# Kernel optimization log

Measured on AMD Instinct MI355X. Metric: run time of the kernel, lower is better.

## Reference

```python
import jax, jax.numpy as jnp
import numpy as np

B, L, SIZE, BACK, H = 4, 1024, 1024, 512, 16
D = SIZE // H  # head_size = 64


def setup_inputs() -> dict:
    key = jax.random.key(0)
    ks = jax.random.split(key, 18)
    s = 0.02
    return {
        "k": jax.random.normal(ks[0], (B, L, SIZE), jnp.float32),
        "v": jax.random.normal(ks[1], (B, L, SIZE), jnp.float32),
        "q": jax.random.normal(ks[2], (B, L, SIZE), jnp.float32),
        "background": jax.random.normal(ks[3], (B, L, BACK), jnp.float32),
        # weights stored [in, out] (pre-transposed vs torch Linear)
        "Wk": jax.random.normal(ks[4], (SIZE, SIZE), jnp.float32) * s,
        "bk": jnp.zeros((SIZE,), jnp.float32),
        "Wv": jax.random.normal(ks[5], (SIZE, SIZE), jnp.float32) * s,
        "bv": jnp.zeros((SIZE,), jnp.float32),
        "Wq": jax.random.normal(ks[6], (SIZE, SIZE), jnp.float32) * s,
        "bq": jnp.zeros((SIZE,), jnp.float32),
        "Wb": jax.random.normal(ks[7], (BACK, SIZE), jnp.float32) * s,
        "bb": jnp.zeros((SIZE,), jnp.float32),
        "Wo": jax.random.normal(ks[8], (SIZE, SIZE), jnp.float32) * s,
        "bo": jnp.zeros((SIZE,), jnp.float32),
    }


def _heads(x):
    # [B, L, H*D] -> [B, H, L, D]
    b, l, _ = x.shape
    return x.reshape(b, l, H, D).transpose(0, 2, 1, 3)


def reference(k, v, q, background, Wk, bk, Wv, bv, Wq, bq, Wb, bb, Wo, bo):
    kh = _heads(k @ Wk + bk)
    vh = _heads(v @ Wv + bv)
    qh = _heads(q @ Wq + bq) / jnp.sqrt(jnp.asarray(D, k.dtype))
    gh = _heads(background @ Wb + bb)
    scores = jnp.einsum("bhqd,bhkd->bhqk", qh, kh)   # [B,H,Lq,Lk]
    gates = jax.nn.sigmoid(jnp.einsum("bhqd,bhkd->bhqk", qh, gh))
    attn = jax.nn.softmax(scores, axis=-1) * gates    # dropout = identity (eval)
    ctx = jnp.einsum("bhqk,bhkd->bhqd", attn, vh)
    ctx = ctx.transpose(0, 2, 1, 3).reshape(k.shape[0], -1, H * D)
    return ctx @ Wo + bo
```

## Files before the change

kernel.cpp:

```cpp
#include <hip/hip_runtime.h>
#include <cstddef>
#include <cstdint>

typedef __attribute__((ext_vector_type(8))) short s16x8;
typedef __attribute__((ext_vector_type(4))) short s16x4;
typedef __attribute__((ext_vector_type(4))) float f32x4;

#define MFMA(a, b, c) __builtin_amdgcn_mfma_f32_16x16x32_bf16(a, b, c, 0, 0, 0)
#define LOG2E 1.44269504088896f

__device__ __forceinline__ short f2bf(float x) {
    uint32_t u = __float_as_uint(x);
    u = (u + 0x7FFFu + ((u >> 16) & 1u)) >> 16;
    return (short)u;
}

__device__ __forceinline__ void gld16(const void* g, void* l) {
    __builtin_amdgcn_global_load_lds(
        (const __attribute__((address_space(1))) unsigned int*)g,
        (__attribute__((address_space(3))) unsigned int*)l, 16, 0, 0);
}

__device__ __forceinline__ float fexp2(float x) {
#if __has_builtin(__builtin_amdgcn_exp2f)
    return __builtin_amdgcn_exp2f(x);
#else
    return exp2f(x);
#endif
}

__device__ __forceinline__ float frcp(float x) {
#if __has_builtin(__builtin_amdgcn_rcpf)
    return __builtin_amdgcn_rcpf(x);
#else
    return 1.f / x;
#endif
}

__device__ __forceinline__ unsigned cvtpk(float lo, float hi) {
    unsigned r;
    asm("v_cvt_pk_bf16_f32 %0, %1, %2" : "=v"(r) : "v"(lo), "v"(hi));
    return r;
}

struct ConvP { const float* in[4]; short* out[4]; };

__global__ __launch_bounds__(256)
void conv_all(ConvP p) {
    const int i = blockIdx.x * 256 + threadIdx.x;
    int r, base;
    if (i < 524288)            { r = 0; base = 0; }
    else if (i < 1048576)      { r = 1; base = 524288; }
    else if (i < 1310720)      { r = 2; base = 1048576; }
    else                       { r = 3; base = 1310720; }
    const int j = i - base;
    const float4 a = *(const float4*)(p.in[r] + (size_t)j * 8);
    const float4 b = *(const float4*)(p.in[r] + (size_t)j * 8 + 4);
    s16x8 o;
    o[0] = f2bf(a.x); o[1] = f2bf(a.y); o[2] = f2bf(a.z); o[3] = f2bf(a.w);
    o[4] = f2bf(b.x); o[5] = f2bf(b.y); o[6] = f2bf(b.z); o[7] = f2bf(b.w);
    *(s16x8*)(p.out[r] + (size_t)j * 8) = o;
}

struct WtP { const float* W[5]; short* Wt[5]; int K[5]; };

__global__ __launch_bounds__(256)
void conv_wt_b(WtP p) {
    __shared__ float T[64][65];
    const int z = blockIdx.z;
    const int K = p.K[z];
    const int k0 = blockIdx.y << 6, n0 = blockIdx.x << 6;
    if (k0 >= K) return;
    const float* W = p.W[z];
    short* Wt = p.Wt[z];
    const int tr = threadIdx.x >> 4, tc4 = (threadIdx.x & 15) << 2;
    #pragma unroll
    for (int i = 0; i < 4; ++i) {
        const int r = tr + i * 16;
        const float4 v = *(const float4*)(W + (size_t)(k0 + r) * 1024 + n0 + tc4);
        T[r][tc4 + 0] = v.x; T[r][tc4 + 1] = v.y;
        T[r][tc4 + 2] = v.z; T[r][tc4 + 3] = v.w;
    }
    __syncthreads();
    #pragma unroll
    for (int i = 0; i < 4; ++i) {
        const int nr = tr + i * 16;
        s16x4 o;
        o[0] = f2bf(T[tc4 + 0][nr]); o[1] = f2bf(T[tc4 + 1][nr]);
        o[2] = f2bf(T[tc4 + 2][nr]); o[3] = f2bf(T[tc4 + 3][nr]);
        *(s16x4*)(Wt + (size_t)(n0 + nr) * K + k0 + tc4) = o;
    }
}

struct Proj5P {
    const short* A[5]; const short* Bt[5]; const float* bias[5];
    void* Y[5]; int Kd[5]; float alpha[5]; int mode[5];
};

__global__ __launch_bounds__(256, 2)
void proj_gemm128d(Proj5P p, int zbase) {
    __shared__ __align__(16) short lds[2 * 16384];

    const int tid = threadIdx.x;
    const int w = tid >> 6, lane = tid & 63;
    const int la = lane & 15, kg = lane >> 4;
    const int wr = w >> 1, wc = w & 1;

    const int cpx = gridDim.x >> 3;
    const int orig = blockIdx.x;
    const int swz = (orig & 7) * cpx + (orig >> 3);
    const int z = zbase + (swz >> 8);
    const int rem = swz & 255;
    const int bm = rem >> 3, bn = rem & 7;

    const short* __restrict__ A  = p.A[z];
    const short* __restrict__ Bt = p.Bt[z];
    const int K = p.Kd[z];
    const int NT = K >> 6;

    const int srow = tid >> 3;
    const int csrc = (tid & 7) ^ (srow & 7);
    const short* gA = A  + (size_t)(bm * 128 + srow) * K + csrc * 8;
    const short* gB = Bt + (size_t)(bn * 128 + srow) * K + csrc * 8;
    short* dstA = &lds[srow * 64 + (tid & 7) * 8];
    short* dstB = dstA + 8192;

#define STAGE(t, nb) do {                                                  \
        const size_t ko_ = (size_t)((t) << 6);                             \
        short* ba_ = dstA + (nb) * 16384;                                  \
        short* bb_ = dstB + (nb) * 16384;                                  \
        _Pragma("unroll")                                                  \
        for (int i = 0; i < 4; ++i) {                                      \
            gld16(gA + (size_t)(32 * i) * K + ko_, ba_ + i * 2048);        \
            gld16(gB + (size_t)(32 * i) * K + ko_, bb_ + i * 2048);       \
        }                                                                  \
    } while (0)

    const int c0 = kg ^ (la & 7), c1 = (4 + kg) ^ (la & 7);
    const int aRd = (wr * 64 + la) * 64;
    const int bRd = 8192 + (wc * 64 + la) * 64;

    f32x4 acc[4][4] = {};

    STAGE(0, 0);
    asm volatile("s_waitcnt vmcnt(0)" ::: "memory");
    asm volatile("s_barrier" ::: "memory");

    for (int t = 0; t < NT; ++t) {
        const int cb = (t & 1) * 16384;
        if (t + 1 < NT) STAGE(t + 1, (t & 1) ^ 1);
        s16x8 af[4][2], bf[4][2];
        #pragma unroll
        for (int m = 0; m < 4; ++m) {
            af[m][0] = *(const s16x8*)&lds[cb + aRd + m * 1024 + c0 * 8];
            af[m][1] = *(const s16x8*)&lds[cb + aRd + m * 1024 + c1 * 8];
        }
        #pragma unroll
        for (int n = 0; n < 4; ++n) {
            bf[n][0] = *(const s16x8*)&lds[cb + bRd + n * 1024 + c0 * 8];
            bf[n][1] = *(const s16x8*)&lds[cb + bRd + n * 1024 + c1 * 8];
        }
        __builtin_amdgcn_s_setprio(1);
        #pragma unroll
        for (int m = 0; m < 4; ++m)
            #pragma unroll
            for (int n = 0; n < 4; ++n) {
                acc[m][n] = MFMA(af[m][0], bf[n][0], acc[m][n]);
                acc[m][n] = MFMA(af[m][1], bf[n][1], acc[m][n]);
            }
        __builtin_amdgcn_s_setprio(0);
        if (t + 1 < NT) {
            asm volatile("s_waitcnt vmcnt(0)" ::: "memory");
            asm volatile("s_barrier" ::: "memory");
        }
    }
#undef STAGE

    const float* __restrict__ bias = p.bias[z];
    const float alpha = p.alpha[z];
    const int mode = p.mode[z];

    if (mode == 2) {
        short* __restrict__ Y = (short*)p.Y[z];
        short* Tv = lds;
        asm volatile("s_waitcnt lgkmcnt(0)" ::: "memory");
        asm volatile("s_barrier" ::: "memory");
        #pragma unroll
        for (int ni = 0; ni < 4; ++ni) {
            const int rrow = wc * 64 + ni * 16 + la;
            const float bs = bias[bn * 128 + rrow];
            #pragma unroll
            for (int mi = 0; mi < 4; ++mi) {
                const int l0 = wr * 64 + mi * 16 + kg * 4;
                const unsigned d0 = cvtpk(alpha * (acc[mi][ni][0] + bs),
                                          alpha * (acc[mi][ni][1] + bs));
                const unsigned d1 = cvtpk(alpha * (acc[mi][ni][2] + bs),
                                          alpha * (acc[mi][ni][3] + bs));
                *(unsigned*)&Tv[rrow * 132 + l0]     = d0;
                *(unsigned*)&Tv[rrow * 132 + l0 + 2] = d1;
            }
        }
        asm volatile("s_barrier" ::: "memory");
        const int bb_ = (bm * 128) >> 10;
        const int l0g = (bm * 128) & 1023;
        #pragma unroll
        for (int s = 0; s < 8; ++s) {
            const int c = tid + (s << 8);
            const int rr = c >> 4, seg = c & 15;
            const int hh = bn * 2 + (rr >> 6), dd = rr & 63;
            const s16x8 vv = *(const s16x8*)&Tv[rr * 132 + seg * 8];
            *(s16x8*)&Y[((((size_t)bb_ * 16 + hh) * 64 + dd) << 10) + l0g + seg * 8] = vv;
        }
        return;
    }

    #pragma unroll
    for (int n = 0; n < 4; ++n) {
        const int col = bn * 128 + wc * 64 + n * 16 + la;
        const float bs = bias[col];
        #pragma unroll
        for (int m = 0; m < 4; ++m) {
            const int row0 = bm * 128 + wr * 64 + m * 16 + kg * 4;
            #pragma unroll
            for (int r = 0; r < 4; ++r) {
                const float v = alpha * (acc[m][n][r] + bs);
                if (mode == 0) {
                    ((short*)p.Y[z])[(size_t)(row0 + r) * 1024 + col] = f2bf(v);
                } else {
                    ((float*)p.Y[z])[(size_t)(row0 + r) * 1024 + col] = v;
                }
            }
        }
    }
}

__global__ __launch_bounds__(512)
void attn_mfma(const short* __restrict__ qh, const short* __restrict__ kh,
               const short* __restrict__ gh, const short* __restrict__ vt,
               short* __restrict__ ctx) {
    __shared__ __align__(16) short lds[33792];

    const int tid = threadIdx.x, w = tid >> 6, lane = tid & 63;
    const int la = lane & 15, kg = lane >> 4;

    const int orig = blockIdx.x;
    const int xcd = orig & 7, i = orig >> 3;
    const int bh = xcd * 8 + (i >> 3);
    const int qt = i & 7;
    const int b = bh >> 4, h = bh & 15;
    const int q0 = qt << 7;

    const size_t hb = ((size_t)b << 20) + ((size_t)h << 6);
    const size_t vtbase = ((size_t)bh) << 16;

    const int qrow = q0 + w * 16 + la;
    const s16x8 aq0 = *(const s16x8*)(qh + hb + (size_t)qrow * 1024 + kg * 8);
    const s16x8 aq1 = *(const s16x8*)(qh + hb + (size_t)qrow * 1024 + 32 + kg * 8);

    const int sr = tid >> 3, sc = tid & 7;
    const int cs = sc ^ (sr & 7);
    const short* ksrc = kh + hb + (size_t)sr * 1024 + cs * 8;
    const short* gsrc = gh + hb + (size_t)sr * 1024 + cs * 8;
    const short* vsrc = vt + vtbase + (size_t)sr * 1024 + cs * 8;
    const int sdst = tid * 8;

    const int ch0 = (kg ^ (la & 7)) * 8;
    const int ch1 = ((4 + kg) ^ (la & 7)) * 8;
    const int pbase = 24576 + w * 1152;

    float s_run = 0.f;
    f32x4 o[4] = {};

#define ASTG(kt, bb) do {                                                  \
        const size_t kr_ = (size_t)((kt) << 6) * 1024;                     \
        gld16(ksrc + kr_, &lds[(bb) * 4096 + sdst]);                       \
        gld16(gsrc + kr_, &lds[8192 + (bb) * 4096 + sdst]);                \
        gld16(vsrc + ((kt) << 6), &lds[16384 + (bb) * 4096 + sdst]);       \
    } while (0)

    ASTG(0, 0);
    asm volatile("s_waitcnt vmcnt(0)" ::: "memory");
    asm volatile("s_barrier" ::: "memory");

    for (int kt = 0; kt < 16; ++kt) {
        const int cb = (kt & 1) * 4096;
        if (kt < 15) ASTG(kt + 1, (kt + 1) & 1);

        f32x4 st[4] = {}, gt[4] = {};
        #pragma unroll
        for (int nf = 0; nf < 4; ++nf) {
            const int rb = cb + (nf * 16 + la) * 64;
            const s16x8 kb0 = *(const s16x8*)&lds[rb + ch0];
            const s16x8 kb1 = *(const s16x8*)&lds[rb + ch1];
            st[nf] = MFMA(kb0, aq0, st[nf]);
            st[nf] = MFMA(kb1, aq1, st[nf]);
            const s16x8 gb0 = *(const s16x8*)&lds[8192 + rb + ch0];
            const s16x8 gb1 = *(const s16x8*)&lds[8192 + rb + ch1];
            gt[nf] = MFMA(gb0, aq0, gt[nf]);
            gt[nf] = MFMA(gb1, aq1, gt[nf]);
        }

        float ps = 0.f;
        unsigned pkw[4][2];
        #pragma unroll
        for (int nf = 0; nf < 4; ++nf) {
            const float p0 = fexp2(st[nf][0]);
            const float p1 = fexp2(st[nf][1]);
            const float p2 = fexp2(st[nf][2]);
            const float p3 = fexp2(st[nf][3]);
            ps += (p0 + p1) + (p2 + p3);
            const float g0 = frcp(1.f + fexp2(-gt[nf][0]));
            const float g1 = frcp(1.f + fexp2(-gt[nf][1]));
            const float g2 = frcp(1.f + fexp2(-gt[nf][2]));
            const float g3 = frcp(1.f + fexp2(-gt[nf][3]));
            pkw[nf][0] = cvtpk(p0 * g0, p1 * g1);
            pkw[nf][1] = cvtpk(p2 * g2, p3 * g3);
        }
        s_run += ps;

        #pragma unroll
        for (int nf = 0; nf < 4; ++nf) {
            *(unsigned*)&lds[pbase + la * 72 + nf * 16 + kg * 4]     = pkw[nf][0];
            *(unsigned*)&lds[pbase + la * 72 + nf * 16 + kg * 4 + 2] = pkw[nf][1];
        }

        const s16x8 pa0 = *(const s16x8*)&lds[pbase + la * 72 + kg * 8];
        const s16x8 pa1 = *(const s16x8*)&lds[pbase + la * 72 + 32 + kg * 8];
        #pragma unroll
        for (int nf = 0; nf < 4; ++nf) {
            const int rb = cb + (nf * 16 + la) * 64;
            const s16x8 vb0 = *(const s16x8*)&lds[16384 + rb + ch0];
            const s16x8 vb1 = *(const s16x8*)&lds[16384 + rb + ch1];
            o[nf] = MFMA(vb0, pa0, o[nf]);
            o[nf] = MFMA(vb1, pa1, o[nf]);
        }

        if (kt < 15) {
            asm volatile("s_waitcnt vmcnt(0)" ::: "memory");
            asm volatile("s_barrier" ::: "memory");
        }
    }
#undef ASTG

    float sv = s_run;
    sv += __shfl_xor(sv, 16);
    sv += __shfl_xor(sv, 32);
    const float inv = frcp(sv);
    short* crow = ctx + ((size_t)(b * 1024 + qrow) << 10) + (h << 6);
    #pragma unroll
    for (int nf = 0; nf < 4; ++nf) {
        *(unsigned*)(crow + nf * 16 + kg * 4)     = cvtpk(o[nf][0] * inv, o[nf][1] * inv);
        *(unsigned*)(crow + nf * 16 + kg * 4 + 2) = cvtpk(o[nf][2] * inv, o[nf][3] * inv);
    }
}

extern "C" void kernel_launch(void* const* d_in, const int* in_sizes, int n_in,
                              void* d_out, int out_size, void* d_ws, size_t ws_size,
                              hipStream_t stream) {
    (void)in_sizes; (void)n_in; (void)out_size; (void)ws_size;

    const float* k  = (const float*)d_in[0];
    const float* v  = (const float*)d_in[1];
    const float* q  = (const float*)d_in[2];
    const float* bg = (const float*)d_in[3];
    const float* Wk = (const float*)d_in[4];  const float* bk = (const float*)d_in[5];
    const float* Wv = (const float*)d_in[6];  const float* bv = (const float*)d_in[7];
    const float* Wq = (const float*)d_in[8];  const float* bq = (const float*)d_in[9];
    const float* Wb = (const float*)d_in[10]; const float* bb = (const float*)d_in[11];
    const float* Wo = (const float*)d_in[12]; const float* bo = (const float*)d_in[13];

    short* ws = (short*)d_ws;
    const size_t MN = (size_t)4096 * 1024;
    short* khb = ws;
    short* qhb = ws + MN;
    short* ghb = ws + 2 * MN;
    short* vtb = ws + 3 * MN;
    short* xk  = ws + 4 * MN;
    short* xq  = ws + 5 * MN;
    short* xg  = ws + 6 * MN;
    short* xv  = ws + 6 * MN + MN / 2;
    short* wkt = ws + 7 * MN + MN / 2;
    short* wvt = wkt + 1048576;
    short* wqt = wvt + 1048576;
    short* wot = wqt + 1048576;
    short* wbt = wot + 1048576;
    short* ctxb = xk;

    const dim3 blk(256);

    WtP wp;
    wp.W[0] = Wk; wp.Wt[0] = wkt; wp.K[0] = 1024;
    wp.W[1] = Wv; wp.Wt[1] = wvt; wp.K[1] = 1024;
    wp.W[2] = Wq; wp.Wt[2] = wqt; wp.K[2] = 1024;
    wp.W[3] = Wb; wp.Wt[3] = wbt; wp.K[3] = 512;
    wp.W[4] = Wo; wp.Wt[4] = wot; wp.K[4] = 1024;
    conv_wt_b<<<dim3(16, 16, 5), blk, 0, stream>>>(wp);

    ConvP cp;
    cp.in[0] = k;  cp.out[0] = xk;
    cp.in[1] = q;  cp.out[1] = xq;
    cp.in[2] = bg; cp.out[2] = xg;
    cp.in[3] = v;  cp.out[3] = xv;
    conv_all<<<7168, blk, 0, stream>>>(cp);

    Proj5P p5;
    p5.A[0] = xk;   p5.Bt[0] = wkt; p5.bias[0] = bk; p5.Y[0] = khb;
    p5.Kd[0] = 1024; p5.alpha[0] = LOG2E;  p5.mode[0] = 0;
    p5.A[1] = xq;   p5.Bt[1] = wqt; p5.bias[1] = bq; p5.Y[1] = qhb;
    p5.Kd[1] = 1024; p5.alpha[1] = 0.125f; p5.mode[1] = 0;
    p5.A[2] = xg;   p5.Bt[2] = wbt; p5.bias[2] = bb; p5.Y[2] = ghb;
    p5.Kd[2] = 512;  p5.alpha[2] = LOG2E;  p5.mode[2] = 0;
    p5.A[3] = xv;   p5.Bt[3] = wvt; p5.bias[3] = bv; p5.Y[3] = vtb;
    p5.Kd[3] = 1024; p5.alpha[3] = 1.0f;   p5.mode[3] = 2;
    p5.A[4] = ctxb; p5.Bt[4] = wot; p5.bias[4] = bo; p5.Y[4] = d_out;
    p5.Kd[4] = 1024; p5.alpha[4] = 1.0f;   p5.mode[4] = 1;

    proj_gemm128d<<<dim3(1024), blk, 0, stream>>>(p5, 0);

    attn_mfma<<<dim3(512), dim3(512), 0, stream>>>(qhb, khb, ghb, vtb, ctxb);

    proj_gemm128d<<<dim3(256), blk, 0, stream>>>(p5, 4);
}
```

Measured before the change: 118.6 us.

## Replace double-buffered K=64 GEMM pipeline with 4-stage K=32 pipeline

The projection GEMM now stages K-tiles of 32 instead of 64 and uses a four-slot LDS ring with three tiles in flight, waiting with partial vmcnt instead of draining all loads each step. The aim is to hide global-to-LDS latency better and avoid a full vmcnt(0) stall per iteration, while keeping total LDS the same. It trades this for twice as many barriers and smaller MFMA batches per barrier, and it changes the LDS swizzle for the 32-wide rows.

```diff
diff --git a/kernel.cpp b/kernel.cpp
--- a/kernel.cpp
+++ b/kernel.cpp
@@ -98,8 +98,8 @@
 };
 
 __global__ __launch_bounds__(256, 2)
-void proj_gemm128d(Proj5P p, int zbase) {
-    __shared__ __align__(16) short lds[2 * 16384];
+void proj_gemm128p(Proj5P p, int zbase) {
+    __shared__ __align__(16) short lds[4 * 8192];
 
     const int tid = threadIdx.x;
     const int w = tid >> 6, lane = tid & 63;
@@ -116,65 +116,63 @@
     const short* __restrict__ A  = p.A[z];
     const short* __restrict__ Bt = p.Bt[z];
     const int K = p.Kd[z];
-    const int NT = K >> 6;
-
-    const int srow = tid >> 3;
-    const int csrc = (tid & 7) ^ (srow & 7);
+    const int NT = K >> 5;
+
+    const int srow = tid >> 2;
+    const int csrc = (tid & 3) ^ ((tid >> 3) & 3);
     const short* gA = A  + (size_t)(bm * 128 + srow) * K + csrc * 8;
     const short* gB = Bt + (size_t)(bn * 128 + srow) * K + csrc * 8;
-    short* dstA = &lds[srow * 64 + (tid & 7) * 8];
-    short* dstB = dstA + 8192;
-
-#define STAGE(t, nb) do {                                                  \
-        const size_t ko_ = (size_t)((t) << 6);                             \
-        short* ba_ = dstA + (nb) * 16384;                                  \
-        short* bb_ = dstB + (nb) * 16384;                                  \
+    const int d0 = tid * 8;
+
+#define STAGE(t) do {                                                      \
+        const int bq_ = ((t) & 3) * 8192;                                  \
+        const size_t ko_ = (size_t)((t) << 5);                             \
+        gld16(gA + ko_,                  &lds[bq_ + d0]);                  \
+        gld16(gA + (size_t)64 * K + ko_, &lds[bq_ + 2048 + d0]);           \
+        gld16(gB + ko_,                  &lds[bq_ + 4096 + d0]);           \
+        gld16(gB + (size_t)64 * K + ko_, &lds[bq_ + 6144 + d0]);           \
+    } while (0)
+
+    const int cr = (kg ^ ((la >> 1) & 3)) * 8;
+    const int aRd = (wr * 64 + la) * 32 + cr;
+    const int bRd = 4096 + (wc * 64 + la) * 32 + cr;
+
+    f32x4 acc[4][4] = {};
+
+#define TILE_BODY(t) do {                                                  \
+        const int cb_ = ((t) & 3) * 8192;                                  \
+        s16x8 af[4], bf[4];                                                \
         _Pragma("unroll")                                                  \
-        for (int i = 0; i < 4; ++i) {                                      \
-            gld16(gA + (size_t)(32 * i) * K + ko_, ba_ + i * 2048);        \
-            gld16(gB + (size_t)(32 * i) * K + ko_, bb_ + i * 2048);       \
-        }                                                                  \
+        for (int m = 0; m < 4; ++m)                                        \
+            af[m] = *(const s16x8*)&lds[cb_ + aRd + m * 512];              \
+        _Pragma("unroll")                                                  \
+        for (int n = 0; n < 4; ++n)                                        \
+            bf[n] = *(const s16x8*)&lds[cb_ + bRd + n * 512];              \
+        __builtin_amdgcn_s_setprio(1);                                     \
+        _Pragma("unroll")                                                  \
+        for (int m = 0; m < 4; ++m)                                        \
+            _Pragma("unroll")                                              \
+            for (int n = 0; n < 4; ++n)                                    \
+                acc[m][n] = MFMA(af[m], bf[n], acc[m][n]);                 \
+        __builtin_amdgcn_s_setprio(0);                                     \
     } while (0)
 
-    const int c0 = kg ^ (la & 7), c1 = (4 + kg) ^ (la & 7);
-    const int aRd = (wr * 64 + la) * 64;
-    const int bRd = 8192 + (wc * 64 + la) * 64;
-
-    f32x4 acc[4][4] = {};
-
-    STAGE(0, 0);
+    STAGE(0); STAGE(1); STAGE(2);
+
+    for (int t = 0; t < NT - 2; ++t) {
+        asm volatile("s_waitcnt vmcnt(8)" ::: "memory");
+        asm volatile("s_barrier" ::: "memory");
+        TILE_BODY(t);
+        if (t + 3 < NT) STAGE(t + 3);
+    }
+    asm volatile("s_waitcnt vmcnt(4)" ::: "memory");
+    asm volatile("s_barrier" ::: "memory");
+    TILE_BODY(NT - 2);
     asm volatile("s_waitcnt vmcnt(0)" ::: "memory");
     asm volatile("s_barrier" ::: "memory");
-
-    for (int t = 0; t < NT; ++t) {
-        const int cb = (t & 1) * 16384;
-        if (t + 1 < NT) STAGE(t + 1, (t & 1) ^ 1);
-        s16x8 af[4][2], bf[4][2];
-        #pragma unroll
-        for (int m = 0; m < 4; ++m) {
-            af[m][0] = *(const s16x8*)&lds[cb + aRd + m * 1024 + c0 * 8];
-            af[m][1] = *(const s16x8*)&lds[cb + aRd + m * 1024 + c1 * 8];
-        }
-        #pragma unroll
-        for (int n = 0; n < 4; ++n) {
-            bf[n][0] = *(const s16x8*)&lds[cb + bRd + n * 1024 + c0 * 8];
-            bf[n][1] = *(const s16x8*)&lds[cb + bRd + n * 1024 + c1 * 8];
-        }
-        __builtin_amdgcn_s_setprio(1);
-        #pragma unroll
-        for (int m = 0; m < 4; ++m)
-            #pragma unroll
-            for (int n = 0; n < 4; ++n) {
-                acc[m][n] = MFMA(af[m][0], bf[n][0], acc[m][n]);
-                acc[m][n] = MFMA(af[m][1], bf[n][1], acc[m][n]);
-            }
-        __builtin_amdgcn_s_setprio(0);
-        if (t + 1 < NT) {
-            asm volatile("s_waitcnt vmcnt(0)" ::: "memory");
-            asm volatile("s_barrier" ::: "memory");
-        }
-    }
+    TILE_BODY(NT - 1);
 #undef STAGE
+#undef TILE_BODY
 
     const float* __restrict__ bias = p.bias[z];
     const float alpha = p.alpha[z];
@@ -192,12 +190,12 @@
             #pragma unroll
             for (int mi = 0; mi < 4; ++mi) {
                 const int l0 = wr * 64 + mi * 16 + kg * 4;
-                const unsigned d0 = cvtpk(alpha * (acc[mi][ni][0] + bs),
-                                          alpha * (acc[mi][ni][1] + bs));
-                const unsigned d1 = cvtpk(alpha * (acc[mi][ni][2] + bs),
-                                          alpha * (acc[mi][ni][3] + bs));
-                *(unsigned*)&Tv[rrow * 132 + l0]     = d0;
-                *(unsigned*)&Tv[rrow * 132 + l0 + 2] = d1;
+                const unsigned dd0 = cvtpk(alpha * (acc[mi][ni][0] + bs),
+                                           alpha * (acc[mi][ni][1] + bs));
+                const unsigned dd1 = cvtpk(alpha * (acc[mi][ni][2] + bs),
+                                           alpha * (acc[mi][ni][3] + bs));
+                *(unsigned*)&Tv[rrow * 132 + l0]     = dd0;
+                *(unsigned*)&Tv[rrow * 132 + l0 + 2] = dd1;
             }
         }
         asm volatile("s_barrier" ::: "memory");
@@ -415,9 +413,9 @@
     p5.A[4] = ctxb; p5.Bt[4] = wot; p5.bias[4] = bo; p5.Y[4] = d_out;
     p5.Kd[4] = 1024; p5.alpha[4] = 1.0f;   p5.mode[4] = 1;
 
-    proj_gemm128d<<<dim3(1024), blk, 0, stream>>>(p5, 0);
+    proj_gemm128p<<<dim3(1024), blk, 0, stream>>>(p5, 0);
 
     attn_mfma<<<dim3(512), dim3(512), 0, stream>>>(qhb, khb, ghb, vtb, ctxb);
 
-    proj_gemm128d<<<dim3(256), blk, 0, stream>>>(p5, 4);
-}
+    proj_gemm128p<<<dim3(256), blk, 0, stream>>>(p5, 4);
+}
```

After: 124.1 us. +4.6%, slower.

## Process 256 query rows per attention block, halving grid and K/G/V reloads

Applied to the files above, without the earlier changes.

Each attention workgroup now handles 256 query rows instead of 128: each wave owns two 16-row query groups, and each K/G/V tile staged in LDS is reused for both. The grid halves from 512 to 256 blocks, so K, G and V are streamed from global memory half as often. The cost is more registers per wave for the doubled accumulators and Q fragments, and only 256 blocks for 256 CUs, so each CU gets about one block with longer serial work and less latency hiding. Launch bounds now request 4 waves per SIMD.

```diff
diff --git a/kernel.cpp b/kernel.cpp
--- a/kernel.cpp
+++ b/kernel.cpp
@@ -234,7 +234,7 @@
     }
 }
 
-__global__ __launch_bounds__(512)
+__global__ __launch_bounds__(512, 4)
 void attn_mfma(const short* __restrict__ qh, const short* __restrict__ kh,
                const short* __restrict__ gh, const short* __restrict__ vt,
                short* __restrict__ ctx) {
@@ -245,17 +245,21 @@
 
     const int orig = blockIdx.x;
     const int xcd = orig & 7, i = orig >> 3;
-    const int bh = xcd * 8 + (i >> 3);
-    const int qt = i & 7;
+    const int bh = xcd * 8 + (i >> 2);
+    const int qt = i & 3;
     const int b = bh >> 4, h = bh & 15;
-    const int q0 = qt << 7;
+    const int q0 = qt << 8;
 
     const size_t hb = ((size_t)b << 20) + ((size_t)h << 6);
     const size_t vtbase = ((size_t)bh) << 16;
 
-    const int qrow = q0 + w * 16 + la;
-    const s16x8 aq0 = *(const s16x8*)(qh + hb + (size_t)qrow * 1024 + kg * 8);
-    const s16x8 aq1 = *(const s16x8*)(qh + hb + (size_t)qrow * 1024 + 32 + kg * 8);
+    s16x8 aq[2][2];
+    #pragma unroll
+    for (int g = 0; g < 2; ++g) {
+        const int qr = q0 + w * 32 + g * 16 + la;
+        aq[g][0] = *(const s16x8*)(qh + hb + (size_t)qr * 1024 + kg * 8);
+        aq[g][1] = *(const s16x8*)(qh + hb + (size_t)qr * 1024 + 32 + kg * 8);
+    }
 
     const int sr = tid >> 3, sc = tid & 7;
     const int cs = sc ^ (sr & 7);
@@ -268,8 +272,8 @@
     const int ch1 = ((4 + kg) ^ (la & 7)) * 8;
     const int pbase = 24576 + w * 1152;
 
-    float s_run = 0.f;
-    f32x4 o[4] = {};
+    float s_run[2] = {0.f, 0.f};
+    f32x4 o[2][4] = {};
 
 #define ASTG(kt, bb) do {                                                  \
         const size_t kr_ = (size_t)((kt) << 6) * 1024;                     \
@@ -286,53 +290,56 @@
         const int cb = (kt & 1) * 4096;
         if (kt < 15) ASTG(kt + 1, (kt + 1) & 1);
 
-        f32x4 st[4] = {}, gt[4] = {};
-        #pragma unroll
-        for (int nf = 0; nf < 4; ++nf) {
-            const int rb = cb + (nf * 16 + la) * 64;
-            const s16x8 kb0 = *(const s16x8*)&lds[rb + ch0];
-            const s16x8 kb1 = *(const s16x8*)&lds[rb + ch1];
-            st[nf] = MFMA(kb0, aq0, st[nf]);
-            st[nf] = MFMA(kb1, aq1, st[nf]);
-            const s16x8 gb0 = *(const s16x8*)&lds[8192 + rb + ch0];
-            const s16x8 gb1 = *(const s16x8*)&lds[8192 + rb + ch1];
-            gt[nf] = MFMA(gb0, aq0, gt[nf]);
-            gt[nf] = MFMA(gb1, aq1, gt[nf]);
-        }
-
-        float ps = 0.f;
-        unsigned pkw[4][2];
-        #pragma unroll
-        for (int nf = 0; nf < 4; ++nf) {
-            const float p0 = fexp2(st[nf][0]);
-            const float p1 = fexp2(st[nf][1]);
-            const float p2 = fexp2(st[nf][2]);
-            const float p3 = fexp2(st[nf][3]);
-            ps += (p0 + p1) + (p2 + p3);
-            const float g0 = frcp(1.f + fexp2(-gt[nf][0]));
-            const float g1 = frcp(1.f + fexp2(-gt[nf][1]));
-            const float g2 = frcp(1.f + fexp2(-gt[nf][2]));
-            const float g3 = frcp(1.f + fexp2(-gt[nf][3]));
-            pkw[nf][0] = cvtpk(p0 * g0, p1 * g1);
-            pkw[nf][1] = cvtpk(p2 * g2, p3 * g3);
-        }
-        s_run += ps;
-
-        #pragma unroll
-        for (int nf = 0; nf < 4; ++nf) {
-            *(unsigned*)&lds[pbase + la * 72 + nf * 16 + kg * 4]     = pkw[nf][0];
-            *(unsigned*)&lds[pbase + la * 72 + nf * 16 + kg * 4 + 2] = pkw[nf][1];
-        }
-
-        const s16x8 pa0 = *(const s16x8*)&lds[pbase + la * 72 + kg * 8];
-        const s16x8 pa1 = *(const s16x8*)&lds[pbase + la * 72 + 32 + kg * 8];
-        #pragma unroll
-        for (int nf = 0; nf < 4; ++nf) {
-            const int rb = cb + (nf * 16 + la) * 64;
-            const s16x8 vb0 = *(const s16x8*)&lds[16384 + rb + ch0];
-            const s16x8 vb1 = *(const s16x8*)&lds[16384 + rb + ch1];
-            o[nf] = MFMA(vb0, pa0, o[nf]);
-            o[nf] = MFMA(vb1, pa1, o[nf]);
+        #pragma unroll
+        for (int g = 0; g < 2; ++g) {
+            f32x4 st[4] = {}, gt[4] = {};
+            #pragma unroll
+            for (int nf = 0; nf < 4; ++nf) {
+                const int rb = cb + (nf * 16 + la) * 64;
+                const s16x8 kb0 = *(const s16x8*)&lds[rb + ch0];
+                const s16x8 kb1 = *(const s16x8*)&lds[rb + ch1];
+                st[nf] = MFMA(kb0, aq[g][0], st[nf]);
+                st[nf] = MFMA(kb1, aq[g][1], st[nf]);
+                const s16x8 gb0 = *(const s16x8*)&lds[8192 + rb + ch0];
+                const s16x8 gb1 = *(const s16x8*)&lds[8192 + rb + ch1];
+                gt[nf] = MFMA(gb0, aq[g][0], gt[nf]);
+                gt[nf] = MFMA(gb1, aq[g][1], gt[nf]);
+            }
+
+            float ps = 0.f;
+            unsigned pkw[4][2];
+            #pragma unroll
+            for (int nf = 0; nf < 4; ++nf) {
+                const float p0 = fexp2(st[nf][0]);
+                const float p1 = fexp2(st[nf][1]);
+                const float p2 = fexp2(st[nf][2]);
+                const float p3 = fexp2(st[nf][3]);
+                ps += (p0 + p1) + (p2 + p3);
+                const float g0 = frcp(1.f + fexp2(-gt[nf][0]));
+                const float g1 = frcp(1.f + fexp2(-gt[nf][1]));
+                const float g2 = frcp(1.f + fexp2(-gt[nf][2]));
+                const float g3 = frcp(1.f + fexp2(-gt[nf][3]));
+                pkw[nf][0] = cvtpk(p0 * g0, p1 * g1);
+                pkw[nf][1] = cvtpk(p2 * g2, p3 * g3);
+            }
+            s_run[g] += ps;
+
+            #pragma unroll
+            for (int nf = 0; nf < 4; ++nf) {
+                *(unsigned*)&lds[pbase + la * 72 + nf * 16 + kg * 4]     = pkw[nf][0];
+                *(unsigned*)&lds[pbase + la * 72 + nf * 16 + kg * 4 + 2] = pkw[nf][1];
+            }
+
+            const s16x8 pa0 = *(const s16x8*)&lds[pbase + la * 72 + kg * 8];
+            const s16x8 pa1 = *(const s16x8*)&lds[pbase + la * 72 + 32 + kg * 8];
+            #pragma unroll
+            for (int nf = 0; nf < 4; ++nf) {
+                const int rb = cb + (nf * 16 + la) * 64;
+                const s16x8 vb0 = *(const s16x8*)&lds[16384 + rb + ch0];
+                const s16x8 vb1 = *(const s16x8*)&lds[16384 + rb + ch1];
+                o[g][nf] = MFMA(vb0, pa0, o[g][nf]);
+                o[g][nf] = MFMA(vb1, pa1, o[g][nf]);
+            }
         }
 
         if (kt < 15) {
@@ -342,15 +349,19 @@
     }
 #undef ASTG
 
-    float sv = s_run;
-    sv += __shfl_xor(sv, 16);
-    sv += __shfl_xor(sv, 32);
-    const float inv = frcp(sv);
-    short* crow = ctx + ((size_t)(b * 1024 + qrow) << 10) + (h << 6);
     #pragma unroll
-    for (int nf = 0; nf < 4; ++nf) {
-        *(unsigned*)(crow + nf * 16 + kg * 4)     = cvtpk(o[nf][0] * inv, o[nf][1] * inv);
-        *(unsigned*)(crow + nf * 16 + kg * 4 + 2) = cvtpk(o[nf][2] * inv, o[nf][3] * inv);
+    for (int g = 0; g < 2; ++g) {
+        float sv = s_run[g];
+        sv += __shfl_xor(sv, 16);
+        sv += __shfl_xor(sv, 32);
+        const float inv = frcp(sv);
+        const int qr = q0 + w * 32 + g * 16 + la;
+        short* crow = ctx + ((size_t)(b * 1024 + qr) << 10) + (h << 6);
+        #pragma unroll
+        for (int nf = 0; nf < 4; ++nf) {
+            *(unsigned*)(crow + nf * 16 + kg * 4)     = cvtpk(o[g][nf][0] * inv, o[g][nf][1] * inv);
+            *(unsigned*)(crow + nf * 16 + kg * 4 + 2) = cvtpk(o[g][nf][2] * inv, o[g][nf][3] * inv);
+        }
     }
 }
 
@@ -417,7 +428,7 @@
 
     proj_gemm128d<<<dim3(1024), blk, 0, stream>>>(p5, 0);
 
-    attn_mfma<<<dim3(512), dim3(512), 0, stream>>>(qhb, khb, ghb, vtb, ctxb);
+    attn_mfma<<<dim3(256), dim3(512), 0, stream>>>(qhb, khb, ghb, vtb, ctxb);
 
     proj_gemm128d<<<dim3(256), blk, 0, stream>>>(p5, 4);
 }
```

Result: slower. 132.9 us (+12.0%).

## Fuse fp32-to-bf16 activation conversion into projection GEMM A-tile staging

Applied to the files above, without the earlier changes.

Removes the standalone conversion kernel that turned the k/q/v/background inputs into bf16 buffers. The projection GEMM now loads fp32 A tiles into registers, packs them to bf16 and writes them to LDS after the wait, while B still uses async global-to-LDS loads. This avoids a full extra read/write pass over the activations, but adds register pressure and serialized conversion and LDS stores in the GEMM main loop, with double the global bytes for the A operand.

```diff
diff --git a/kernel.cpp b/kernel.cpp
--- a/kernel.cpp
+++ b/kernel.cpp
@@ -5,6 +5,7 @@
 typedef __attribute__((ext_vector_type(8))) short s16x8;
 typedef __attribute__((ext_vector_type(4))) short s16x4;
 typedef __attribute__((ext_vector_type(4))) float f32x4;
+typedef __attribute__((ext_vector_type(4))) unsigned u32x4;
 
 #define MFMA(a, b, c) __builtin_amdgcn_mfma_f32_16x16x32_bf16(a, b, c, 0, 0, 0)
 #define LOG2E 1.44269504088896f
@@ -41,25 +42,6 @@
     unsigned r;
     asm("v_cvt_pk_bf16_f32 %0, %1, %2" : "=v"(r) : "v"(lo), "v"(hi));
     return r;
-}
-
-struct ConvP { const float* in[4]; short* out[4]; };
-
-__global__ __launch_bounds__(256)
-void conv_all(ConvP p) {
-    const int i = blockIdx.x * 256 + threadIdx.x;
-    int r, base;
-    if (i < 524288)            { r = 0; base = 0; }
-    else if (i < 1048576)      { r = 1; base = 524288; }
-    else if (i < 1310720)      { r = 2; base = 1048576; }
-    else                       { r = 3; base = 1310720; }
-    const int j = i - base;
-    const float4 a = *(const float4*)(p.in[r] + (size_t)j * 8);
-    const float4 b = *(const float4*)(p.in[r] + (size_t)j * 8 + 4);
-    s16x8 o;
-    o[0] = f2bf(a.x); o[1] = f2bf(a.y); o[2] = f2bf(a.z); o[3] = f2bf(a.w);
-    o[4] = f2bf(b.x); o[5] = f2bf(b.y); o[6] = f2bf(b.z); o[7] = f2bf(b.w);
-    *(s16x8*)(p.out[r] + (size_t)j * 8) = o;
 }
 
 struct WtP { const float* W[5]; short* Wt[5]; int K[5]; };
@@ -93,10 +75,13 @@
 }
 
 struct Proj5P {
-    const short* A[5]; const short* Bt[5]; const float* bias[5];
+    const float* Af[5];
+    const short* A[5];
+    const short* Bt[5]; const float* bias[5];
     void* Y[5]; int Kd[5]; float alpha[5]; int mode[5];
 };
 
+template <int F32A>
 __global__ __launch_bounds__(256, 2)
 void proj_gemm128d(Proj5P p, int zbase) {
     __shared__ __align__(16) short lds[2 * 16384];
@@ -113,26 +98,46 @@
     const int rem = swz & 255;
     const int bm = rem >> 3, bn = rem & 7;
 
-    const short* __restrict__ A  = p.A[z];
-    const short* __restrict__ Bt = p.Bt[z];
     const int K = p.Kd[z];
     const int NT = K >> 6;
 
     const int srow = tid >> 3;
     const int csrc = (tid & 7) ^ (srow & 7);
-    const short* gA = A  + (size_t)(bm * 128 + srow) * K + csrc * 8;
-    const short* gB = Bt + (size_t)(bn * 128 + srow) * K + csrc * 8;
+    const float* gAf = p.Af[z] ? p.Af[z] + (size_t)(bm * 128 + srow) * K + csrc * 8 : nullptr;
+    const short* gA  = p.A[z]  ? p.A[z]  + (size_t)(bm * 128 + srow) * K + csrc * 8 : nullptr;
+    const short* gB  = p.Bt[z] + (size_t)(bn * 128 + srow) * K + csrc * 8;
     short* dstA = &lds[srow * 64 + (tid & 7) * 8];
     short* dstB = dstA + 8192;
 
-#define STAGE(t, nb) do {                                                  \
+    float4 av[4][2];
+
+#define STAGE_ISSUE(t, nb) do {                                            \
         const size_t ko_ = (size_t)((t) << 6);                             \
-        short* ba_ = dstA + (nb) * 16384;                                  \
         short* bb_ = dstB + (nb) * 16384;                                  \
         _Pragma("unroll")                                                  \
         for (int i = 0; i < 4; ++i) {                                      \
-            gld16(gA + (size_t)(32 * i) * K + ko_, ba_ + i * 2048);        \
-            gld16(gB + (size_t)(32 * i) * K + ko_, bb_ + i * 2048);       \
+            if (F32A) {                                                    \
+                av[i][0] = *(const float4*)(gAf + (size_t)(32 * i) * K + ko_);     \
+                av[i][1] = *(const float4*)(gAf + (size_t)(32 * i) * K + ko_ + 4); \
+            } else {                                                       \
+                gld16(gA + (size_t)(32 * i) * K + ko_,                     \
+                      dstA + (nb) * 16384 + i * 2048);                     \
+            }                                                              \
+            gld16(gB + (size_t)(32 * i) * K + ko_, bb_ + i * 2048);        \
+        }                                                                  \
+    } while (0)
+
+#define A_WRITE(nb) do {                                                   \
+        if (F32A) {                                                        \
+            _Pragma("unroll")                                              \
+            for (int i = 0; i < 4; ++i) {                                  \
+                u32x4 pk;                                                  \
+                pk[0] = cvtpk(av[i][0].x, av[i][0].y);                     \
+                pk[1] = cvtpk(av[i][0].z, av[i][0].w);                     \
+                pk[2] = cvtpk(av[i][1].x, av[i][1].y);                     \
+                pk[3] = cvtpk(av[i][1].z, av[i][1].w);                     \
+                *(u32x4*)(dstA + (nb) * 16384 + i * 2048) = pk;            \
+            }                                                              \
         }                                                                  \
     } while (0)
 
@@ -142,13 +147,16 @@
 
     f32x4 acc[4][4] = {};
 
-    STAGE(0, 0);
+    STAGE_ISSUE(0, 0);
     asm volatile("s_waitcnt vmcnt(0)" ::: "memory");
+    A_WRITE(0);
+    asm volatile("s_waitcnt lgkmcnt(0)" ::: "memory");
     asm volatile("s_barrier" ::: "memory");
 
     for (int t = 0; t < NT; ++t) {
         const int cb = (t & 1) * 16384;
-        if (t + 1 < NT) STAGE(t + 1, (t & 1) ^ 1);
+        const int nb = (t & 1) ^ 1;
+        if (t + 1 < NT) STAGE_ISSUE(t + 1, nb);
         s16x8 af[4][2], bf[4][2];
         #pragma unroll
         for (int m = 0; m < 4; ++m) {
@@ -171,10 +179,13 @@
         __builtin_amdgcn_s_setprio(0);
         if (t + 1 < NT) {
             asm volatile("s_waitcnt vmcnt(0)" ::: "memory");
+            A_WRITE(nb);
+            asm volatile("s_waitcnt lgkmcnt(0)" ::: "memory");
             asm volatile("s_barrier" ::: "memory");
         }
     }
-#undef STAGE
+#undef STAGE_ISSUE
+#undef A_WRITE
 
     const float* __restrict__ bias = p.bias[z];
     const float alpha = p.alpha[z];
@@ -200,6 +211,7 @@
                 *(unsigned*)&Tv[rrow * 132 + l0 + 2] = d1;
             }
         }
+        asm volatile("s_waitcnt lgkmcnt(0)" ::: "memory");
         asm volatile("s_barrier" ::: "memory");
         const int bb_ = (bm * 128) >> 10;
         const int l0g = (bm * 128) & 1023;
@@ -371,20 +383,16 @@
 
     short* ws = (short*)d_ws;
     const size_t MN = (size_t)4096 * 1024;
-    short* khb = ws;
-    short* qhb = ws + MN;
-    short* ghb = ws + 2 * MN;
-    short* vtb = ws + 3 * MN;
-    short* xk  = ws + 4 * MN;
-    short* xq  = ws + 5 * MN;
-    short* xg  = ws + 6 * MN;
-    short* xv  = ws + 6 * MN + MN / 2;
-    short* wkt = ws + 7 * MN + MN / 2;
-    short* wvt = wkt + 1048576;
-    short* wqt = wvt + 1048576;
-    short* wot = wqt + 1048576;
-    short* wbt = wot + 1048576;
-    short* ctxb = xk;
+    short* khb  = ws;
+    short* qhb  = ws + MN;
+    short* ghb  = ws + 2 * MN;
+    short* vtb  = ws + 3 * MN;
+    short* ctxb = ws + 4 * MN;
+    short* wkt  = ws + 5 * MN;
+    short* wvt  = wkt + 1048576;
+    short* wqt  = wvt + 1048576;
+    short* wot  = wqt + 1048576;
+    short* wbt  = wot + 1048576;
 
     const dim3 blk(256);
 
@@ -396,28 +404,19 @@
     wp.W[4] = Wo; wp.Wt[4] = wot; wp.K[4] = 1024;
     conv_wt_b<<<dim3(16, 16, 5), blk, 0, stream>>>(wp);
 
-    ConvP cp;
-    cp.in[0] = k;  cp.out[0] = xk;
-    cp.in[1] = q;  cp.out[1] = xq;
-    cp.in[2] = bg; cp.out[2] = xg;
-    cp.in[3] = v;  cp.out[3] = xv;
-    conv_all<<<7168, blk, 0, stream>>>(cp);
-
     Proj5P p5;
-    p5.A[0] = xk;   p5.Bt[0] = wkt; p5.bias[0] = bk; p5.Y[0] = khb;
-    p5.Kd[0] = 1024; p5.alpha[0] = LOG2E;  p5.mode[0] = 0;
-    p5.A[1] = xq;   p5.Bt[1] = wqt; p5.bias[1] = bq; p5.Y[1] = qhb;
-    p5.Kd[1] = 1024; p5.alpha[1] = 0.125f; p5.mode[1] = 0;
-    p5.A[2] = xg;   p5.Bt[2] = wbt; p5.bias[2] = bb; p5.Y[2] = ghb;
-    p5.Kd[2] = 512;  p5.alpha[2] = LOG2E;  p5.mode[2] = 0;
-    p5.A[3] = xv;   p5.Bt[3] = wvt; p5.bias[3] = bv; p5.Y[3] = vtb;
-    p5.Kd[3] = 1024; p5.alpha[3] = 1.0f;   p5.mode[3] = 2;
-    p5.A[4] = ctxb; p5.Bt[4] = wot; p5.bias[4] = bo; p5.Y[4] = d_out;
-    p5.Kd[4] = 1024; p5.alpha[4] = 1.0f;   p5.mode[4] = 1;
-
-    proj_gemm128d<<<dim3(1024), blk, 0, stream>>>(p5, 0);
-
+    p5.Af[0] = k;  p5.A[0] = nullptr; p5.Bt[0] = wkt; p5.bias[0] = bk;
+    p5.Y[0] = khb; p5.Kd[0] = 1024; p5.alpha[0] = LOG2E;  p5.mode[0] = 0;
+    p5.Af[1] = q;  p5.A[1] = nullptr; p5.Bt[1] = wqt; p5.bias[1] = bq;
+    p5.Y[1] = qhb; p5.Kd[1] = 1024; p5.alpha[1] = 0.125f; p5.mode[1] = 0;
+    p5.Af[2] = bg; p5.A[2] = nullptr; p5.Bt[2] = wbt; p5.bias[2] = bb;
+    p5.Y[2] = ghb; p5.Kd[2] = 512;  p5.alpha[2] = LOG2E;  p5.mode[2] = 0;
+    p5.Af[3] = v;  p5.A[3] = nullptr; p5.Bt[3] = wvt; p5.bias[3] = bv;
+    p5.Y[3] = vtb; p5.Kd[3] = 1024; p5.alpha[3] = 1.0f;   p5.mode[3] = 2;
+    p5.Af[4] = nullptr; p5.A[4] = ctxb; p5.Bt[4] = wot; p5.bias[4] = bo;
+    p5.Y[4] = d_out; p5.Kd[4] = 1024; p5.alpha[4] = 1.0f; p5.mode[4] = 1;
+
+    proj_gemm128d<1><<<dim3(1024), blk, 0, stream>>>(p5, 0);
     attn_mfma<<<dim3(512), dim3(512), 0, stream>>>(qhb, khb, ghb, vtb, ctxb);
-
-    proj_gemm128d<<<dim3(256), blk, 0, stream>>>(p5, 4);
-}
+    proj_gemm128d<0><<<dim3(256), blk, 0, stream>>>(p5, 4);
+}
```

New measurement: 116.0 us. 1.02x faster.
